# Performance work log

Hardware: AMD Instinct MI355X
Metric: run time of the kernel (lower is better)

The kernel has to match this reference:

```python
import jax, jax.numpy as jnp
import numpy as np

B, S, D, E, H = 2, 1024, 1024, 8, 3584
Z_COEF = 1e-3
LOAD_COEF = 1e-3


def setup_inputs() -> dict:
    key = jax.random.key(0)
    k = jax.random.split(key, 5)
    x = jax.random.normal(k[0], (B, S, D), dtype=jnp.float32)
    Wr = jax.random.normal(k[1], (E, D), dtype=jnp.float32) / np.sqrt(D)   # router: Linear(D, E) weight [out,in]
    W1 = jax.random.normal(k[2], (E, H, D), dtype=jnp.float32) / np.sqrt(D)  # per-expert w1 [out=H,in=D]
    W2 = jax.random.normal(k[3], (E, H, D), dtype=jnp.float32) / np.sqrt(D)  # per-expert w2
    W3 = jax.random.normal(k[4], (E, D, H), dtype=jnp.float32) / np.sqrt(H)  # per-expert w3 [out=D,in=H]
    return {"x": x, "Wr": Wr, "W1": W1, "W2": W2, "W3": W3}


def reference(x, Wr, W1, W2, W3):
    b, s, d = x.shape
    e = Wr.shape[0]
    # Router
    router_logits = jnp.einsum('bsd,ed->bse', x, Wr)            # [B,S,E]
    probs = jax.nn.softmax(router_logits, axis=-1)
    topk_probs, topk_idx = jax.lax.top_k(probs, 1)              # top_k = 1 (see notes)
    # Dense one-hot dispatch (faithful to original einsum dispatch)
    flat_x = x.reshape(-1, d)                                   # [N,D]
    flat_idx = topk_idx.reshape(-1)                             # [N]
    mask = jax.nn.one_hot(flat_idx, e, dtype=x.dtype)           # [N,E]
    xin = jnp.einsum('ne,nd->end', mask, flat_x)                # [E,N,D] masked expert inputs
    # All experts over all tokens (SwiGLU), batched over E
    h = jax.nn.silu(jnp.einsum('end,ehd->enh', xin, W1)) * jnp.einsum('end,ehd->enh', xin, W2)
    out_e = jnp.einsum('enh,edh->end', h, W3)                   # [E,N,D]
    # Combine with the 0/1 mask (original does NOT weight by topk_probs)
    out = jnp.einsum('end,ne->nd', out_e, mask).reshape(b, s, d)
    # dropout p=0 -> identity
    # Aux losses
    z_loss = jnp.mean(jax.nn.logsumexp(router_logits, axis=-1)) ** 2
    expert_load = probs.sum(axis=0)                             # [S,E] (sum over dim 0, as in torch)
    load_loss = (jnp.std(expert_load, ddof=1) / jnp.mean(expert_load)) ** 2
    aux_loss = Z_COEF * z_loss + LOAD_COEF * load_loss
    return out, aux_loss
```

## Files before the change

### kernel.cpp

```cpp
#include <hip/hip_runtime.h>
#include <hip/hip_bf16.h>
#include <math.h>


#define NB 2
#define NS 1024
#define ND 1024
#define NE 8
#define NH 3584
#define NTOK 2048
#define LDK 72

typedef float f32x4 __attribute__((ext_vector_type(4)));
typedef __bf16 bf16x8 __attribute__((ext_vector_type(8)));
typedef unsigned short u16x4 __attribute__((ext_vector_type(4)));
typedef unsigned int u32x4 __attribute__((ext_vector_type(4)));

__device__ __forceinline__ unsigned short f2bf(float f) {
  unsigned int u = __builtin_bit_cast(unsigned int, f);
  u = (u + 0x7fffu + ((u >> 16) & 1u)) >> 16;
  return (unsigned short)u;
}
__device__ __forceinline__ float bf2f(unsigned short s) {
  unsigned int u = ((unsigned int)s) << 16;
  return __builtin_bit_cast(float, u);
}

__global__ __launch_bounds__(256) void router_kernel(
    const float* __restrict__ x, const float* __restrict__ Wr,
    float* __restrict__ probs, float* __restrict__ lse,
    int* __restrict__ counts, int* __restrict__ expert_of)
{
  int n = blockIdx.x;
  int t = threadIdx.x;
  const float* xr = x + (size_t)n * ND;
  float xv[4];
#pragma unroll
  for (int j = 0; j < 4; ++j) xv[j] = xr[t + j * 256];
  float p[NE];
#pragma unroll
  for (int e = 0; e < NE; ++e) p[e] = 0.f;
#pragma unroll
  for (int j = 0; j < 4; ++j) {
    int d = t + j * 256;
#pragma unroll
    for (int e = 0; e < NE; ++e) p[e] += xv[j] * Wr[e * ND + d];
  }
#pragma unroll
  for (int e = 0; e < NE; ++e) {
#pragma unroll
    for (int o = 32; o > 0; o >>= 1) p[e] += __shfl_down(p[e], o, 64);
  }
  __shared__ float red[4][NE];
  int wid = t >> 6, lane = t & 63;
  if (lane == 0) {
#pragma unroll
    for (int e = 0; e < NE; ++e) red[wid][e] = p[e];
  }
  __syncthreads();
  if (t == 0) {
    float lg[NE];
#pragma unroll
    for (int e = 0; e < NE; ++e) lg[e] = red[0][e] + red[1][e] + red[2][e] + red[3][e];
    float m = lg[0]; int arg = 0;
#pragma unroll
    for (int e = 1; e < NE; ++e) if (lg[e] > m) { m = lg[e]; arg = e; }
    float s = 0.f, ex[NE];
#pragma unroll
    for (int e = 0; e < NE; ++e) { ex[e] = expf(lg[e] - m); s += ex[e]; }
    float inv = 1.f / s;
#pragma unroll
    for (int e = 0; e < NE; ++e) probs[n * NE + e] = ex[e] * inv;
    lse[n] = m + logf(s);
    expert_of[n] = arg;
    atomicAdd(&counts[arg], 1);
  }
}

__global__ __launch_bounds__(256) void aux_offsets_kernel(
    const float* __restrict__ probs, const float* __restrict__ lse,
    const int* __restrict__ counts, int* __restrict__ offsets,
    int* __restrict__ cursors, float* __restrict__ out_aux)
{
  int t = threadIdx.x;
  float lsum = 0.f;
  for (int n = t; n < NTOK; n += 256) lsum += lse[n];
  float esum = 0.f, esq = 0.f;
  for (int i = t; i < NS * NE; i += 256) {
    float v = probs[i] + probs[NS * NE + i];
    esum += v; esq += v * v;
  }
  __shared__ float rb[3][4];
  int wid = t >> 6, lane = t & 63;
#pragma unroll
  for (int o = 32; o > 0; o >>= 1) {
    lsum += __shfl_down(lsum, o, 64);
    esum += __shfl_down(esum, o, 64);
    esq  += __shfl_down(esq, o, 64);
  }
  if (lane == 0) { rb[0][wid] = lsum; rb[1][wid] = esum; rb[2][wid] = esq; }
  __syncthreads();
  if (t == 0) {
    lsum = rb[0][0] + rb[0][1] + rb[0][2] + rb[0][3];
    esum = rb[1][0] + rb[1][1] + rb[1][2] + rb[1][3];
    esq  = rb[2][0] + rb[2][1] + rb[2][2] + rb[2][3];
    float zmean = lsum / (float)NTOK;
    float z_loss = zmean * zmean;
    const float nn = (float)(NS * NE);
    float mean = esum / nn;
    float var = (esq - esum * esum / nn) / (nn - 1.0f);
    float load_loss = var / (mean * mean);
    out_aux[0] = 1e-3f * z_loss + 1e-3f * load_loss;
    int off = 0;
#pragma unroll
    for (int e = 0; e < NE; ++e) { offsets[e] = off; cursors[e] = off; off += counts[e]; }
    offsets[NE] = off;
  }
}

__global__ __launch_bounds__(256) void scatter_kernel(
    const int* __restrict__ expert_of, int* __restrict__ cursors,
    int* __restrict__ token_list)
{
  int n = blockIdx.x * 256 + threadIdx.x;
  int e = expert_of[n];
  int p = atomicAdd(&cursors[e], 1);
  token_list[p] = n;
}

__global__ __launch_bounds__(256, 2) void moe_gemm12(
    const float* __restrict__ x, const float* __restrict__ W1f,
    const float* __restrict__ W2f, const int* __restrict__ offsets,
    const int* __restrict__ token_list, unsigned short* __restrict__ h)
{
  int e = blockIdx.z;
  int base = offsets[e], cnt = offsets[e + 1] - base;
  int m0 = blockIdx.y * 128;
  if (m0 >= cnt) return;
  int n0 = blockIdx.x * 64;
  const float* B1 = W1f + (size_t)e * ((size_t)NH * ND) + (size_t)n0 * ND;
  const float* B2 = W2f + (size_t)e * ((size_t)NH * ND) + (size_t)n0 * ND;

  __shared__ __align__(16) unsigned short As[2][128][LDK];
  __shared__ __align__(16) unsigned short B1s[2][64][LDK];
  __shared__ __align__(16) unsigned short B2s[2][64][LDK];
  __shared__ int rowtok[128];

  int t = threadIdx.x;
  if (t < 128) {
    int mc = m0 + t; if (mc > cnt - 1) mc = cnt - 1;
    rowtok[t] = token_list[base + mc];
  }
  __syncthreads();

  int rsub = t >> 4;
  int c4 = (t & 15) * 4;

  const float* asrc[8];
#pragma unroll
  for (int rr = 0; rr < 8; ++rr)
    asrc[rr] = x + (size_t)rowtok[rr * 16 + rsub] * ND + c4;
  const float* b1src = B1 + (size_t)rsub * ND + c4;
  const float* b2src = B2 + (size_t)rsub * ND + c4;

  f32x4 ra[8], rb1[4], rb2[4];

  auto load_step = [&](int k0) {
#pragma unroll
    for (int rr = 0; rr < 8; ++rr) ra[rr] = *(const f32x4*)(asrc[rr] + k0);
#pragma unroll
    for (int rr = 0; rr < 4; ++rr) {
      rb1[rr] = *(const f32x4*)(b1src + (size_t)rr * 16 * ND + k0);
      rb2[rr] = *(const f32x4*)(b2src + (size_t)rr * 16 * ND + k0);
    }
  };
  auto store_buf = [&](int buf) {
#pragma unroll
    for (int rr = 0; rr < 8; ++rr) {
      u16x4 p;
      p[0] = f2bf(ra[rr][0]); p[1] = f2bf(ra[rr][1]);
      p[2] = f2bf(ra[rr][2]); p[3] = f2bf(ra[rr][3]);
      *(u16x4*)&As[buf][rr * 16 + rsub][c4] = p;
    }
#pragma unroll
    for (int rr = 0; rr < 4; ++rr) {
      u16x4 p, q;
      p[0] = f2bf(rb1[rr][0]); p[1] = f2bf(rb1[rr][1]);
      p[2] = f2bf(rb1[rr][2]); p[3] = f2bf(rb1[rr][3]);
      q[0] = f2bf(rb2[rr][0]); q[1] = f2bf(rb2[rr][1]);
      q[2] = f2bf(rb2[rr][2]); q[3] = f2bf(rb2[rr][3]);
      *(u16x4*)&B1s[buf][rr * 16 + rsub][c4] = p;
      *(u16x4*)&B2s[buf][rr * 16 + rsub][c4] = q;
    }
  };

  int lane = t & 63, wid = t >> 6;
  int wm = (wid >> 1) * 64;
  int wn = (wid & 1) * 32;
  int rl = lane & 15;
  int ksel = (lane >> 4) * 8;

  f32x4 acc1[4][2] = {}, acc2[4][2] = {};

  load_step(0);
  store_buf(0);
  __syncthreads();

  const int NSTEP = ND / 64;
  for (int ks = 0; ks < NSTEP; ++ks) {
    int cur = ks & 1;
    bool more = (ks + 1) < NSTEP;
    if (more) load_step((ks + 1) * 64);
#pragma unroll
    for (int kk = 0; kk < 2; ++kk) {
      int klo = kk * 32 + ksel;
      bf16x8 af[4], b1[2], b2[2];
#pragma unroll
      for (int i = 0; i < 4; ++i) af[i] = *(const bf16x8*)&As[cur][wm + i * 16 + rl][klo];
#pragma unroll
      for (int j = 0; j < 2; ++j) {
        b1[j] = *(const bf16x8*)&B1s[cur][wn + j * 16 + rl][klo];
        b2[j] = *(const bf16x8*)&B2s[cur][wn + j * 16 + rl][klo];
      }
#pragma unroll
      for (int i = 0; i < 4; ++i)
#pragma unroll
        for (int j = 0; j < 2; ++j) {
          acc1[i][j] = __builtin_amdgcn_mfma_f32_16x16x32_bf16(af[i], b1[j], acc1[i][j], 0, 0, 0);
          acc2[i][j] = __builtin_amdgcn_mfma_f32_16x16x32_bf16(af[i], b2[j], acc2[i][j], 0, 0, 0);
        }
    }
    if (more) store_buf(cur ^ 1);
    __syncthreads();
  }

  int rq = lane >> 4;
#pragma unroll
  for (int i = 0; i < 4; ++i)
#pragma unroll
    for (int r = 0; r < 4; ++r) {
      int mrow = wm + i * 16 + rq * 4 + r;
      int m = m0 + mrow;
      if (m < cnt) {
#pragma unroll
        for (int j = 0; j < 2; ++j) {
          int col = n0 + wn + j * 16 + rl;
          float g1 = acc1[i][j][r], g2 = acc2[i][j][r];
          float hv = g1 / (1.f + expf(-g1)) * g2;
          h[(size_t)(base + m) * NH + col] = f2bf(hv);
        }
      }
    }
}

__global__ __launch_bounds__(256, 2) void moe_gemm3(
    const unsigned short* __restrict__ h, const float* __restrict__ W3f,
    const int* __restrict__ offsets, const int* __restrict__ token_list,
    float* __restrict__ out)
{
  int e = blockIdx.z;
  int base = offsets[e], cnt = offsets[e + 1] - base;
  int m0 = blockIdx.y * 128;
  if (m0 >= cnt) return;
  int n0 = blockIdx.x * 64;
  const float* B = W3f + (size_t)e * ((size_t)ND * NH) + (size_t)n0 * NH;

  __shared__ __align__(16) unsigned short As[2][128][LDK];
  __shared__ __align__(16) unsigned short Bs[2][64][LDK];
  __shared__ int rowtok[128];

  int t = threadIdx.x;
  if (t < 128) {
    int mc = m0 + t; if (mc > cnt - 1) mc = cnt - 1;
    rowtok[t] = token_list[base + mc];
  }
  __syncthreads();

  int rsub8 = t >> 3;
  int c8 = (t & 7) * 8;
  const unsigned short* asrc[4];
#pragma unroll
  for (int rr = 0; rr < 4; ++rr) {
    int row = rr * 32 + rsub8;
    int mc = m0 + row; if (mc > cnt - 1) mc = cnt - 1;
    asrc[rr] = h + (size_t)(base + mc) * NH + c8;
  }
  int rsub = t >> 4;
  int c4 = (t & 15) * 4;
  const float* bsrc = B + (size_t)rsub * NH + c4;

  u32x4 ra[4];
  f32x4 rb[4];
  auto load_step = [&](int k0) {
#pragma unroll
    for (int rr = 0; rr < 4; ++rr) ra[rr] = *(const u32x4*)(asrc[rr] + k0);
#pragma unroll
    for (int rr = 0; rr < 4; ++rr) rb[rr] = *(const f32x4*)(bsrc + (size_t)rr * 16 * NH + k0);
  };
  auto store_buf = [&](int buf) {
#pragma unroll
    for (int rr = 0; rr < 4; ++rr) *(u32x4*)&As[buf][rr * 32 + rsub8][c8] = ra[rr];
#pragma unroll
    for (int rr = 0; rr < 4; ++rr) {
      u16x4 p;
      p[0] = f2bf(rb[rr][0]); p[1] = f2bf(rb[rr][1]);
      p[2] = f2bf(rb[rr][2]); p[3] = f2bf(rb[rr][3]);
      *(u16x4*)&Bs[buf][rr * 16 + rsub][c4] = p;
    }
  };

  int lane = t & 63, wid = t >> 6;
  int wm = (wid >> 1) * 64;
  int wn = (wid & 1) * 32;
  int rl = lane & 15;
  int ksel = (lane >> 4) * 8;

  f32x4 acc[4][2] = {};

  load_step(0);
  store_buf(0);
  __syncthreads();

  const int NSTEP = NH / 64;
  for (int ks = 0; ks < NSTEP; ++ks) {
    int cur = ks & 1;
    bool more = (ks + 1) < NSTEP;
    if (more) load_step((ks + 1) * 64);
#pragma unroll
    for (int kk = 0; kk < 2; ++kk) {
      int klo = kk * 32 + ksel;
      bf16x8 af[4], bv[2];
#pragma unroll
      for (int i = 0; i < 4; ++i) af[i] = *(const bf16x8*)&As[cur][wm + i * 16 + rl][klo];
#pragma unroll
      for (int j = 0; j < 2; ++j) bv[j] = *(const bf16x8*)&Bs[cur][wn + j * 16 + rl][klo];
#pragma unroll
      for (int i = 0; i < 4; ++i)
#pragma unroll
        for (int j = 0; j < 2; ++j)
          acc[i][j] = __builtin_amdgcn_mfma_f32_16x16x32_bf16(af[i], bv[j], acc[i][j], 0, 0, 0);
    }
    if (more) store_buf(cur ^ 1);
    __syncthreads();
  }

  int rq = lane >> 4;
#pragma unroll
  for (int i = 0; i < 4; ++i)
#pragma unroll
    for (int r = 0; r < 4; ++r) {
      int mrow = wm + i * 16 + rq * 4 + r;
      int m = m0 + mrow;
      if (m < cnt) {
        int tok = rowtok[mrow];
#pragma unroll
        for (int j = 0; j < 2; ++j) {
          int col = n0 + wn + j * 16 + rl;
          out[(size_t)tok * ND + col] = acc[i][j][r];
        }
      }
    }
}

extern "C" void kernel_launch(void* const* d_in, const int* in_sizes, int n_in,
                              void* d_out, int out_size, void* d_ws, size_t ws_size,
                              hipStream_t stream)
{
  (void)in_sizes; (void)n_in; (void)out_size; (void)ws_size;
  const float* x  = (const float*)d_in[0];
  const float* Wr = (const float*)d_in[1];
  const float* W1 = (const float*)d_in[2];
  const float* W2 = (const float*)d_in[3];
  const float* W3 = (const float*)d_in[4];
  float* out = (float*)d_out;

  char* w = (char*)d_ws;
  float* probs    = (float*)(w + 0);
  float* lse      = (float*)(w + 65536);
  int* counts     = (int*)(w + 73728);
  int* cursors    = (int*)(w + 73760);
  int* offsets    = (int*)(w + 73792);
  int* expert_of  = (int*)(w + 73856);
  int* token_list = (int*)(w + 82048);
  unsigned short* h = (unsigned short*)(w + 131072);

  hipMemsetAsync(counts, 0, 32, stream);
  router_kernel<<<NTOK, 256, 0, stream>>>(x, Wr, probs, lse, counts, expert_of);
  aux_offsets_kernel<<<1, 256, 0, stream>>>(probs, lse, counts, offsets, cursors,
                                            out + (size_t)NTOK * ND);
  scatter_kernel<<<NTOK / 256, 256, 0, stream>>>(expert_of, cursors, token_list);
  moe_gemm12<<<dim3(NH / 64, NTOK / 128, NE), 256, 0, stream>>>(
      x, W1, W2, offsets, token_list, h);
  moe_gemm3<<<dim3(ND / 64, NTOK / 128, NE), 256, 0, stream>>>(
      h, W3, offsets, token_list, out);
}
```

Measured before the change: 243.5 us.

## Split-K gemm3 with atomics, two-register-set prefetch pipeline, native bf16 converts

The down-projection GEMM is split into two K halves. Each half accumulates into the zero-initialised output with float atomicAdd, which doubles the block count and improves occupancy for the small per-expert M. Both GEMMs now hold two register sets so global loads run two K-steps ahead of the MFMA work. The manual rounding bf16 conversion is replaced by the compiler's native __bf16 cast. The costs are an extra memset of the output, atomic traffic, higher register pressure, and nondeterministic summation order.

```diff
diff --git a/kernel.cpp b/kernel.cpp
--- a/kernel.cpp
+++ b/kernel.cpp
@@ -16,15 +16,17 @@
 typedef unsigned short u16x4 __attribute__((ext_vector_type(4)));
 typedef unsigned int u32x4 __attribute__((ext_vector_type(4)));
 
-__device__ __forceinline__ unsigned short f2bf(float f) {
-  unsigned int u = __builtin_bit_cast(unsigned int, f);
-  u = (u + 0x7fffu + ((u >> 16) & 1u)) >> 16;
-  return (unsigned short)u;
-}
-__device__ __forceinline__ float bf2f(unsigned short s) {
-  unsigned int u = ((unsigned int)s) << 16;
-  return __builtin_bit_cast(float, u);
-}
+__device__ __forceinline__ u16x4 cvt4(f32x4 v) {
+  u16x4 r;
+  r[0] = __builtin_bit_cast(unsigned short, (__bf16)v[0]);
+  r[1] = __builtin_bit_cast(unsigned short, (__bf16)v[1]);
+  r[2] = __builtin_bit_cast(unsigned short, (__bf16)v[2]);
+  r[3] = __builtin_bit_cast(unsigned short, (__bf16)v[3]);
+  return r;
+}
+
+struct R12 { f32x4 a[8]; f32x4 b1[4]; f32x4 b2[4]; };
+struct R3  { u32x4 a[4]; f32x4 b[4]; };
 
 __global__ __launch_bounds__(256) void router_kernel(
     const float* __restrict__ x, const float* __restrict__ Wr,
@@ -163,34 +165,23 @@
   const float* b1src = B1 + (size_t)rsub * ND + c4;
   const float* b2src = B2 + (size_t)rsub * ND + c4;
 
-  f32x4 ra[8], rb1[4], rb2[4];
-
-  auto load_step = [&](int k0) {
-#pragma unroll
-    for (int rr = 0; rr < 8; ++rr) ra[rr] = *(const f32x4*)(asrc[rr] + k0);
+  auto load12 = [&](R12& r, int k0) {
+#pragma unroll
+    for (int rr = 0; rr < 8; ++rr) r.a[rr] = *(const f32x4*)(asrc[rr] + k0);
 #pragma unroll
     for (int rr = 0; rr < 4; ++rr) {
-      rb1[rr] = *(const f32x4*)(b1src + (size_t)rr * 16 * ND + k0);
-      rb2[rr] = *(const f32x4*)(b2src + (size_t)rr * 16 * ND + k0);
-    }
-  };
-  auto store_buf = [&](int buf) {
-#pragma unroll
-    for (int rr = 0; rr < 8; ++rr) {
-      u16x4 p;
-      p[0] = f2bf(ra[rr][0]); p[1] = f2bf(ra[rr][1]);
-      p[2] = f2bf(ra[rr][2]); p[3] = f2bf(ra[rr][3]);
-      *(u16x4*)&As[buf][rr * 16 + rsub][c4] = p;
-    }
+      r.b1[rr] = *(const f32x4*)(b1src + (size_t)rr * 16 * ND + k0);
+      r.b2[rr] = *(const f32x4*)(b2src + (size_t)rr * 16 * ND + k0);
+    }
+  };
+  auto store12 = [&](int buf, const R12& r) {
+#pragma unroll
+    for (int rr = 0; rr < 8; ++rr)
+      *(u16x4*)&As[buf][rr * 16 + rsub][c4] = cvt4(r.a[rr]);
 #pragma unroll
     for (int rr = 0; rr < 4; ++rr) {
-      u16x4 p, q;
-      p[0] = f2bf(rb1[rr][0]); p[1] = f2bf(rb1[rr][1]);
-      p[2] = f2bf(rb1[rr][2]); p[3] = f2bf(rb1[rr][3]);
-      q[0] = f2bf(rb2[rr][0]); q[1] = f2bf(rb2[rr][1]);
-      q[2] = f2bf(rb2[rr][2]); q[3] = f2bf(rb2[rr][3]);
-      *(u16x4*)&B1s[buf][rr * 16 + rsub][c4] = p;
-      *(u16x4*)&B2s[buf][rr * 16 + rsub][c4] = q;
+      *(u16x4*)&B1s[buf][rr * 16 + rsub][c4] = cvt4(r.b1[rr]);
+      *(u16x4*)&B2s[buf][rr * 16 + rsub][c4] = cvt4(r.b2[rr]);
     }
   };
 
@@ -202,25 +193,17 @@
 
   f32x4 acc1[4][2] = {}, acc2[4][2] = {};
 
-  load_step(0);
-  store_buf(0);
-  __syncthreads();
-
-  const int NSTEP = ND / 64;
-  for (int ks = 0; ks < NSTEP; ++ks) {
-    int cur = ks & 1;
-    bool more = (ks + 1) < NSTEP;
-    if (more) load_step((ks + 1) * 64);
+  auto mfma12 = [&](int buf) {
 #pragma unroll
     for (int kk = 0; kk < 2; ++kk) {
       int klo = kk * 32 + ksel;
       bf16x8 af[4], b1[2], b2[2];
 #pragma unroll
-      for (int i = 0; i < 4; ++i) af[i] = *(const bf16x8*)&As[cur][wm + i * 16 + rl][klo];
+      for (int i = 0; i < 4; ++i) af[i] = *(const bf16x8*)&As[buf][wm + i * 16 + rl][klo];
 #pragma unroll
       for (int j = 0; j < 2; ++j) {
-        b1[j] = *(const bf16x8*)&B1s[cur][wn + j * 16 + rl][klo];
-        b2[j] = *(const bf16x8*)&B2s[cur][wn + j * 16 + rl][klo];
+        b1[j] = *(const bf16x8*)&B1s[buf][wn + j * 16 + rl][klo];
+        b2[j] = *(const bf16x8*)&B2s[buf][wn + j * 16 + rl][klo];
       }
 #pragma unroll
       for (int i = 0; i < 4; ++i)
@@ -230,7 +213,23 @@
           acc2[i][j] = __builtin_amdgcn_mfma_f32_16x16x32_bf16(af[i], b2[j], acc2[i][j], 0, 0, 0);
         }
     }
-    if (more) store_buf(cur ^ 1);
+  };
+
+  R12 r0, r1;
+  load12(r0, 0);
+  load12(r1, 64);
+  store12(0, r0);
+  __syncthreads();
+
+  const int NSTEP = ND / 64;
+  for (int ks = 0; ks < NSTEP; ks += 2) {
+    if (ks + 2 < NSTEP) load12(r0, (ks + 2) * 64);
+    mfma12(0);
+    store12(1, r1);
+    __syncthreads();
+    if (ks + 3 < NSTEP) load12(r1, (ks + 3) * 64);
+    mfma12(1);
+    if (ks + 2 < NSTEP) store12(0, r0);
     __syncthreads();
   }
 
@@ -247,7 +246,7 @@
           int col = n0 + wn + j * 16 + rl;
           float g1 = acc1[i][j][r], g2 = acc2[i][j][r];
           float hv = g1 / (1.f + expf(-g1)) * g2;
-          h[(size_t)(base + m) * NH + col] = f2bf(hv);
+          h[(size_t)(base + m) * NH + col] = __builtin_bit_cast(unsigned short, (__bf16)hv);
         }
       }
     }
@@ -262,8 +261,10 @@
   int base = offsets[e], cnt = offsets[e + 1] - base;
   int m0 = blockIdx.y * 128;
   if (m0 >= cnt) return;
-  int n0 = blockIdx.x * 64;
-  const float* B = W3f + (size_t)e * ((size_t)ND * NH) + (size_t)n0 * NH;
+  int n0 = (blockIdx.x >> 1) * 64;
+  int kc = blockIdx.x & 1;
+  const int KOFF = kc * (NH / 2);
+  const float* B = W3f + (size_t)e * ((size_t)ND * NH) + (size_t)n0 * NH + KOFF;
 
   __shared__ __align__(16) unsigned short As[2][128][LDK];
   __shared__ __align__(16) unsigned short Bs[2][64][LDK];
@@ -283,30 +284,24 @@
   for (int rr = 0; rr < 4; ++rr) {
     int row = rr * 32 + rsub8;
     int mc = m0 + row; if (mc > cnt - 1) mc = cnt - 1;
-    asrc[rr] = h + (size_t)(base + mc) * NH + c8;
+    asrc[rr] = h + (size_t)(base + mc) * NH + KOFF + c8;
   }
   int rsub = t >> 4;
   int c4 = (t & 15) * 4;
   const float* bsrc = B + (size_t)rsub * NH + c4;
 
-  u32x4 ra[4];
-  f32x4 rb[4];
-  auto load_step = [&](int k0) {
-#pragma unroll
-    for (int rr = 0; rr < 4; ++rr) ra[rr] = *(const u32x4*)(asrc[rr] + k0);
-#pragma unroll
-    for (int rr = 0; rr < 4; ++rr) rb[rr] = *(const f32x4*)(bsrc + (size_t)rr * 16 * NH + k0);
-  };
-  auto store_buf = [&](int buf) {
-#pragma unroll
-    for (int rr = 0; rr < 4; ++rr) *(u32x4*)&As[buf][rr * 32 + rsub8][c8] = ra[rr];
-#pragma unroll
-    for (int rr = 0; rr < 4; ++rr) {
-      u16x4 p;
-      p[0] = f2bf(rb[rr][0]); p[1] = f2bf(rb[rr][1]);
-      p[2] = f2bf(rb[rr][2]); p[3] = f2bf(rb[rr][3]);
-      *(u16x4*)&Bs[buf][rr * 16 + rsub][c4] = p;
-    }
+  auto load3 = [&](R3& r, int k0) {
+#pragma unroll
+    for (int rr = 0; rr < 4; ++rr) r.a[rr] = *(const u32x4*)(asrc[rr] + k0);
+#pragma unroll
+    for (int rr = 0; rr < 4; ++rr) r.b[rr] = *(const f32x4*)(bsrc + (size_t)rr * 16 * NH + k0);
+  };
+  auto store3 = [&](int buf, const R3& r) {
+#pragma unroll
+    for (int rr = 0; rr < 4; ++rr) *(u32x4*)&As[buf][rr * 32 + rsub8][c8] = r.a[rr];
+#pragma unroll
+    for (int rr = 0; rr < 4; ++rr)
+      *(u16x4*)&Bs[buf][rr * 16 + rsub][c4] = cvt4(r.b[rr]);
   };
 
   int lane = t & 63, wid = t >> 6;
@@ -317,30 +312,38 @@
 
   f32x4 acc[4][2] = {};
 
-  load_step(0);
-  store_buf(0);
-  __syncthreads();
-
-  const int NSTEP = NH / 64;
-  for (int ks = 0; ks < NSTEP; ++ks) {
-    int cur = ks & 1;
-    bool more = (ks + 1) < NSTEP;
-    if (more) load_step((ks + 1) * 64);
+  auto mfma3 = [&](int buf) {
 #pragma unroll
     for (int kk = 0; kk < 2; ++kk) {
       int klo = kk * 32 + ksel;
       bf16x8 af[4], bv[2];
 #pragma unroll
-      for (int i = 0; i < 4; ++i) af[i] = *(const bf16x8*)&As[cur][wm + i * 16 + rl][klo];
-#pragma unroll
-      for (int j = 0; j < 2; ++j) bv[j] = *(const bf16x8*)&Bs[cur][wn + j * 16 + rl][klo];
+      for (int i = 0; i < 4; ++i) af[i] = *(const bf16x8*)&As[buf][wm + i * 16 + rl][klo];
+#pragma unroll
+      for (int j = 0; j < 2; ++j) bv[j] = *(const bf16x8*)&Bs[buf][wn + j * 16 + rl][klo];
 #pragma unroll
       for (int i = 0; i < 4; ++i)
 #pragma unroll
         for (int j = 0; j < 2; ++j)
           acc[i][j] = __builtin_amdgcn_mfma_f32_16x16x32_bf16(af[i], bv[j], acc[i][j], 0, 0, 0);
     }
-    if (more) store_buf(cur ^ 1);
+  };
+
+  R3 r0, r1;
+  load3(r0, 0);
+  load3(r1, 64);
+  store3(0, r0);
+  __syncthreads();
+
+  const int NSTEP = (NH / 2) / 64;
+  for (int ks = 0; ks < NSTEP; ks += 2) {
+    if (ks + 2 < NSTEP) load3(r0, (ks + 2) * 64);
+    mfma3(0);
+    store3(1, r1);
+    __syncthreads();
+    if (ks + 3 < NSTEP) load3(r1, (ks + 3) * 64);
+    mfma3(1);
+    if (ks + 2 < NSTEP) store3(0, r0);
     __syncthreads();
   }
 
@@ -356,7 +359,7 @@
 #pragma unroll
         for (int j = 0; j < 2; ++j) {
           int col = n0 + wn + j * 16 + rl;
-          out[(size_t)tok * ND + col] = acc[i][j][r];
+          atomicAdd(&out[(size_t)tok * ND + col], acc[i][j][r]);
         }
       }
     }
@@ -385,12 +388,13 @@
   unsigned short* h = (unsigned short*)(w + 131072);
 
   hipMemsetAsync(counts, 0, 32, stream);
+  hipMemsetAsync(out, 0, (size_t)NTOK * ND * sizeof(float), stream);
   router_kernel<<<NTOK, 256, 0, stream>>>(x, Wr, probs, lse, counts, expert_of);
   aux_offsets_kernel<<<1, 256, 0, stream>>>(probs, lse, counts, offsets, cursors,
                                             out + (size_t)NTOK * ND);
   scatter_kernel<<<NTOK / 256, 256, 0, stream>>>(expert_of, cursors, token_list);
   moe_gemm12<<<dim3(NH / 64, NTOK / 128, NE), 256, 0, stream>>>(
       x, W1, W2, offsets, token_list, h);
-  moe_gemm3<<<dim3(ND / 64, NTOK / 128, NE), 256, 0, stream>>>(
+  moe_gemm3<<<dim3((ND / 64) * 2, NTOK / 128, NE), 256, 0, stream>>>(
       h, W3, offsets, token_list, out);
 }
```

Measured after the change: 351.2 us. +44.3%, slower.
